# Kernel tuning notes

Measured on AMD Instinct MI355X. Metric: run time of the kernel, lower is better.

The kernel has to match this reference:

```python
import jax, jax.numpy as jnp
from jax import lax
import numpy as np

B, T, K = 256, 512, 256
MAX_SEQ = 512  # max_sequence_length; output padded to MAX_SEQ + 2


def setup_inputs() -> dict:
    key = jax.random.key(0)
    k1, k2 = jax.random.split(key)
    emissions = jax.random.normal(k1, (B, T, K), dtype=jnp.float32)
    transitions = jax.random.normal(k2, (K, K), dtype=jnp.float32)
    mask = jnp.ones((B, T), dtype=jnp.int32)  # prefix mask; here full-length
    return {"emissions": emissions, "transitions": transitions, "mask": mask,
            "max_sequence_length": MAX_SEQ}


def _crf_decode(emissions, transitions, mask):
    # emissions: [B, T, K] float; transitions: [K, K]; mask: [B, T] int (prefix 1s)
    b, t, k = emissions.shape
    state0 = emissions[:, 0, :]                      # [B, K]
    em_rest = jnp.swapaxes(emissions[:, 1:, :], 0, 1)  # [T-1, B, K]
    mk_rest = jnp.swapaxes(mask[:, 1:], 0, 1)           # [T-1, B]

    def fwd(state, xs):
        em_t, mk_t = xs
        # scores[b, i, j] = state[b, i] + transitions[i, j]  (prev tag i -> cur tag j)
        scores = state[:, :, None] + transitions[None, :, :]   # [B, K, K]
        bp = jnp.argmax(scores, axis=1).astype(jnp.int32)       # [B, K] best prev tag
        new_state = jnp.max(scores, axis=1) + em_t              # [B, K]
        valid = (mk_t > 0)[:, None]
        # RNN-with-mask semantics: keep last valid state past sequence end
        return jnp.where(valid, new_state, state), bp

    last_state, bps = lax.scan(fwd, state0, (em_rest, mk_rest))  # bps: [T-1, B, K]
    last_tag = jnp.argmax(last_state, axis=-1).astype(jnp.int32)  # [B]

    def bwd(tag, xs):
        bp_t, mk_t = xs
        out = tag  # tag at this timestep
        prev = jnp.take_along_axis(bp_t, tag[:, None], axis=1)[:, 0]
        tag = jnp.where(mk_t > 0, prev, tag)  # only step back on valid positions
        return tag, out

    tag0, outs = lax.scan(bwd, last_tag, (bps, mk_rest), reverse=True)
    # outs[t] = tag at position t+1 (t = 0..T-2); tag0 = tag at position 0
    tags = jnp.concatenate([tag0[:, None], jnp.swapaxes(outs, 0, 1)], axis=1)  # [B, T]
    return tags


def reference(emissions, transitions, mask, max_sequence_length):
    tags = _crf_decode(emissions, transitions, mask)
    tags = tags * mask  # zero out padding positions
    pad = max_sequence_length + 2 - tags.shape[1]
    return jnp.pad(tags, ((0, 0), (0, pad)))
```

## Files before the change

kernel.cpp:

```cpp
#include <hip/hip_runtime.h>


#define TK 256
#define TT 512

typedef float v2f __attribute__((ext_vector_type(2)));
typedef float v4f __attribute__((ext_vector_type(4)));

__device__ __forceinline__ float max3f(float a, float b, float c) {
  float d;
  asm("v_max3_f32 %0, %1, %2, %3" : "=v"(d) : "v"(a), "v"(b), "v"(c));
  return d;
}

__global__ void transpose_kernel(const float* __restrict__ trans,
                                 float* __restrict__ transT) {
  int j = blockIdx.x;
  int i = threadIdx.x;
  transT[(size_t)j * TK + i] = trans[(size_t)i * TK + j];
}

#define K16(X) X(0) X(1) X(2) X(3) X(4) X(5) X(6) X(7) \
               X(8) X(9) X(10) X(11) X(12) X(13) X(14) X(15)

__global__ __launch_bounds__(1024)
__attribute__((amdgpu_waves_per_eu(4, 4)))
void crf_fwd(const float* __restrict__ em,
             const float* __restrict__ transT,
             const int* __restrict__ mask,
             float* __restrict__ states) {
  const int b = blockIdx.x;
  const int tid = threadIdx.x;
  const int lane = tid & 63;
  const int w = tid >> 6;
  const int g = w >> 1;
  const int p = w & 1;
  const int j0 = 128 * p + 2 * lane;

  __shared__ __align__(16) float st_w[16][32];
  __shared__ float part[2][8][2][2][64];
  __shared__ int mk[TT];

  const float* ta = transT + (size_t)j0 * TK + 32 * g;
  const float* tbq = ta + TK;
#define TRD(n) \
  const v2f TA##n = *reinterpret_cast<const v2f*>(ta + 2 * (n)); \
  const v2f TB##n = *reinterpret_cast<const v2f*>(tbq + 2 * (n));
  K16(TRD)
#undef TRD

  if (tid < TT) mk[tid] = mask[(size_t)b * TT + tid];

  const size_t base = (size_t)b * TT * TK;
  const int pj = g >> 2;
  const int sel = lane & 1;
  const int col = 16 * (g & 3) + (lane >> 1);

  float ns = 0.f, e1 = 0.f, e2 = 0.f;
  if (lane < 32) {
    ns = em[base + 32 * g + lane];
    st_w[w][lane] = ns;
    if (p == 0) states[base + 32 * g + lane] = ns;
    e1 = em[base + TK + 32 * g + lane];
    e2 = em[base + 2 * TK + 32 * g + lane];
  }
  __syncthreads();

  const float* emp = em + base + 3 * TK + 32 * g + lane;
  float* stg = states + base + TK + 32 * g + lane;
  const float* sw = st_w[w];

  for (int t = 1; t < TT; ++t) {
    const v4f S0 = reinterpret_cast<const v4f*>(sw)[0];
    const v4f S1 = reinterpret_cast<const v4f*>(sw)[1];
    const v4f S2 = reinterpret_cast<const v4f*>(sw)[2];
    const v4f S3 = reinterpret_cast<const v4f*>(sw)[3];
    const v4f S4 = reinterpret_cast<const v4f*>(sw)[4];
    const v4f S5 = reinterpret_cast<const v4f*>(sw)[5];
    const v4f S6 = reinterpret_cast<const v4f*>(sw)[6];
    const v4f S7 = reinterpret_cast<const v4f*>(sw)[7];

    float ax, ay;
    {
      const float c0 = S0.x + TA0.x, c1 = S0.y + TA0.y;
      ax = fmaxf(c0, c1);
      const float d0 = S0.x + TB0.x, d1 = S0.y + TB0.y;
      ay = fmaxf(d0, d1);
    }
#define STEP2(Sa, Sb, TAn, TBn)                                   \
    {                                                             \
      const float c0 = Sa + TAn.x, c1 = Sb + TAn.y;               \
      ax = max3f(ax, c0, c1);                                     \
      const float d0 = Sa + TBn.x, d1 = Sb + TBn.y;               \
      ay = max3f(ay, d0, d1);                                     \
    }
    STEP2(S0.z, S0.w, TA1, TB1)
    STEP2(S1.x, S1.y, TA2, TB2)
    STEP2(S1.z, S1.w, TA3, TB3)
    STEP2(S2.x, S2.y, TA4, TB4)
    STEP2(S2.z, S2.w, TA5, TB5)
    STEP2(S3.x, S3.y, TA6, TB6)
    STEP2(S3.z, S3.w, TA7, TB7)
    STEP2(S4.x, S4.y, TA8, TB8)
    STEP2(S4.z, S4.w, TA9, TB9)
    STEP2(S5.x, S5.y, TA10, TB10)
    STEP2(S5.z, S5.w, TA11, TB11)
    STEP2(S6.x, S6.y, TA12, TB12)
    STEP2(S6.z, S6.w, TA13, TB13)
    STEP2(S7.x, S7.y, TA14, TB14)
    STEP2(S7.z, S7.w, TA15, TB15)
#undef STEP2

    float* pw = &part[t & 1][g][p][0][lane];
    pw[0] = ax;
    pw[64] = ay;

    __builtin_amdgcn_sched_barrier(0);
    asm volatile("s_waitcnt lgkmcnt(0)" ::: "memory");
    __builtin_amdgcn_s_barrier();
    __builtin_amdgcn_sched_barrier(0);

    if (lane < 32) {
      const float* pf = &part[t & 1][0][pj][sel][col];
      const float f0 = pf[0];
      const float f1 = pf[256];
      const float f2 = pf[512];
      const float f3 = pf[768];
      const float f4 = pf[1024];
      const float f5 = pf[1280];
      const float f6 = pf[1536];
      const float f7 = pf[1792];
      float f = max3f(fmaxf(f0, f1), f2, f3);
      f = max3f(f, f4, f5);
      f = max3f(f, f6, f7);
      ns = (mk[t] > 0) ? (f + e1) : ns;
      st_w[w][lane] = ns;
      if (p == 0) *stg = ns;
      stg += TK;
      e1 = e2;
      if (t + 2 < TT) e2 = *emp;
      emp += TK;
    }
  }
}

__device__ __forceinline__ float wave_max(float m) {
#pragma unroll
  for (int d = 1; d < 64; d <<= 1) m = fmaxf(m, __shfl_xor(m, d, 64));
  return m;
}

__device__ __forceinline__ int first_eq_idx(float s0, float s1, float s2,
                                            float s3, float m) {
  unsigned long long b0 = __ballot(s0 == m);
  unsigned long long b1 = __ballot(s1 == m);
  unsigned long long b2 = __ballot(s2 == m);
  unsigned long long b3 = __ballot(s3 == m);
  int best = 0x7fffffff;
  if (b0) best = min(best, 4 * (__ffsll(b0) - 1) + 0);
  if (b1) best = min(best, 4 * (__ffsll(b1) - 1) + 1);
  if (b2) best = min(best, 4 * (__ffsll(b2) - 1) + 2);
  if (b3) best = min(best, 4 * (__ffsll(b3) - 1) + 3);
  return best;
}

__global__ __launch_bounds__(64, 1) void crf_bwd(const float* __restrict__ states,
                                                 const float* __restrict__ transT,
                                                 const int* __restrict__ mask,
                                                 int* __restrict__ out,
                                                 int out_stride) {
  const int b = blockIdx.x;
  const int lane = threadIdx.x;

  __shared__ int mk[TT];
  for (int q = lane; q < TT; q += 64) mk[q] = mask[(size_t)b * TT + q];
  __syncthreads();

  const size_t sbase = (size_t)b * TT * TK;
  int* outp = out + (size_t)b * out_stride;

  for (int q = TT + lane; q < out_stride; q += 64) outp[q] = 0;

  const float* srow = states + sbase;
  float4 r = *reinterpret_cast<const float4*>(srow + (size_t)(TT - 1) * TK + 4 * lane);
  float lm = fmaxf(fmaxf(r.x, r.y), fmaxf(r.z, r.w));
  lm = wave_max(lm);
  int tag = first_eq_idx(r.x, r.y, r.z, r.w, lm);

  auto LOADROW = [&](int rr) -> float4 {
    return *reinterpret_cast<const float4*>(srow + (size_t)rr * TK + 4 * lane);
  };
  float4 p0 = LOADROW(TT - 2), p1 = LOADROW(TT - 3), p2 = LOADROW(TT - 4),
         p3 = LOADROW(TT - 5);

  auto STEP = [&](float4 pr, int t) {
    int mkt = mk[t];
    if (lane == 0) outp[t] = (mkt > 0) ? tag : 0;
    const float4 tv =
        *reinterpret_cast<const float4*>(transT + (size_t)tag * TK + 4 * lane);
    float s0 = pr.x + tv.x;
    float s1 = pr.y + tv.y;
    float s2 = pr.z + tv.z;
    float s3 = pr.w + tv.w;
    float m = fmaxf(fmaxf(s0, s1), fmaxf(s2, s3));
    m = wave_max(m);
    int prev = first_eq_idx(s0, s1, s2, s3, m);
    tag = (mkt > 0) ? prev : tag;
  };

  int t = TT - 1;
  while (t >= 4) {
    STEP(p0, t);     if (t - 5 >= 0) p0 = LOADROW(t - 5);
    STEP(p1, t - 1); if (t - 6 >= 0) p1 = LOADROW(t - 6);
    STEP(p2, t - 2); if (t - 7 >= 0) p2 = LOADROW(t - 7);
    STEP(p3, t - 3); if (t - 8 >= 0) p3 = LOADROW(t - 8);
    t -= 4;
  }
  STEP(p0, 3);
  STEP(p1, 2);
  STEP(p2, 1);
  if (lane == 0) outp[0] = (mk[0] > 0) ? tag : 0;
}

extern "C" void kernel_launch(void* const* d_in, const int* in_sizes, int n_in,
                              void* d_out, int out_size, void* d_ws, size_t ws_size,
                              hipStream_t stream) {
  const float* em = (const float*)d_in[0];
  const float* trans = (const float*)d_in[1];
  const int* mask = (const int*)d_in[2];
  int* out = (int*)d_out;

  const int B = in_sizes[0] / (TT * TK);
  const int out_stride = out_size / B;

  float* states = (float*)d_ws;
  float* transT = states + (size_t)B * TT * TK;

  transpose_kernel<<<TK, TK, 0, stream>>>(trans, transT);
  crf_fwd<<<B, 1024, 0, stream>>>(em, transT, mask, states);
  crf_bwd<<<B, 64, 0, stream>>>(states, transT, mask, out, out_stride);
}
```

Before: 794.4 us.

## Fuse CRF forward scan and backtrack into a single kernel

Merges the forward Viterbi kernel and the backtracking kernel into one launch: after the forward loop, wave 0 of each block does the backtrack over the states it just wrote, reusing the mask already staged in LDS. This removes a kernel launch and the gap between the two kernels, and may let the backtrack read recently written states from cache. It also drops the sched_barrier fences around the step barrier and rewrites the max3 inline asm as an accumulate form. The trade-off is that a 1024-thread block stays resident while only one wave does the serial backtrack, and the compiler is now freer to reorder around the barrier.

Result: no change. 794.3 us (-0.0%).

```diff
diff --git a/kernel.cpp b/kernel.cpp
--- a/kernel.cpp
+++ b/kernel.cpp
@@ -7,10 +7,8 @@
 typedef float v2f __attribute__((ext_vector_type(2)));
 typedef float v4f __attribute__((ext_vector_type(4)));
 
-__device__ __forceinline__ float max3f(float a, float b, float c) {
-  float d;
-  asm("v_max3_f32 %0, %1, %2, %3" : "=v"(d) : "v"(a), "v"(b), "v"(c));
-  return d;
+__device__ __forceinline__ void max3acc(float& acc, float a, float b) {
+  asm("v_max3_f32 %0, %0, %1, %2" : "+v"(acc) : "v"(a), "v"(b));
 }
 
 __global__ void transpose_kernel(const float* __restrict__ trans,
@@ -20,15 +18,34 @@
   transT[(size_t)j * TK + i] = trans[(size_t)i * TK + j];
 }
 
-#define K16(X) X(0) X(1) X(2) X(3) X(4) X(5) X(6) X(7) \
-               X(8) X(9) X(10) X(11) X(12) X(13) X(14) X(15)
+__device__ __forceinline__ float wave_max(float m) {
+#pragma unroll
+  for (int d = 1; d < 64; d <<= 1) m = fmaxf(m, __shfl_xor(m, d, 64));
+  return m;
+}
+
+__device__ __forceinline__ int first_eq_idx(float s0, float s1, float s2,
+                                            float s3, float m) {
+  unsigned long long b0 = __ballot(s0 == m);
+  unsigned long long b1 = __ballot(s1 == m);
+  unsigned long long b2 = __ballot(s2 == m);
+  unsigned long long b3 = __ballot(s3 == m);
+  int best = 0x7fffffff;
+  if (b0) best = min(best, 4 * (__ffsll(b0) - 1) + 0);
+  if (b1) best = min(best, 4 * (__ffsll(b1) - 1) + 1);
+  if (b2) best = min(best, 4 * (__ffsll(b2) - 1) + 2);
+  if (b3) best = min(best, 4 * (__ffsll(b3) - 1) + 3);
+  return best;
+}
 
 __global__ __launch_bounds__(1024)
 __attribute__((amdgpu_waves_per_eu(4, 4)))
-void crf_fwd(const float* __restrict__ em,
-             const float* __restrict__ transT,
-             const int* __restrict__ mask,
-             float* __restrict__ states) {
+void crf_fused(const float* __restrict__ em,
+               const float* __restrict__ transT,
+               const int* __restrict__ mask,
+               float* __restrict__ states,
+               int* __restrict__ out,
+               int out_stride) {
   const int b = blockIdx.x;
   const int tid = threadIdx.x;
   const int lane = tid & 63;
@@ -43,11 +60,14 @@
 
   const float* ta = transT + (size_t)j0 * TK + 32 * g;
   const float* tbq = ta + TK;
+#define K16(X) X(0) X(1) X(2) X(3) X(4) X(5) X(6) X(7) \
+               X(8) X(9) X(10) X(11) X(12) X(13) X(14) X(15)
 #define TRD(n) \
   const v2f TA##n = *reinterpret_cast<const v2f*>(ta + 2 * (n)); \
   const v2f TB##n = *reinterpret_cast<const v2f*>(tbq + 2 * (n));
   K16(TRD)
 #undef TRD
+#undef K16
 
   if (tid < TT) mk[tid] = mask[(size_t)b * TT + tid];
 
@@ -71,14 +91,15 @@
   const float* sw = st_w[w];
 
   for (int t = 1; t < TT; ++t) {
-    const v4f S0 = reinterpret_cast<const v4f*>(sw)[0];
-    const v4f S1 = reinterpret_cast<const v4f*>(sw)[1];
-    const v4f S2 = reinterpret_cast<const v4f*>(sw)[2];
-    const v4f S3 = reinterpret_cast<const v4f*>(sw)[3];
-    const v4f S4 = reinterpret_cast<const v4f*>(sw)[4];
-    const v4f S5 = reinterpret_cast<const v4f*>(sw)[5];
-    const v4f S6 = reinterpret_cast<const v4f*>(sw)[6];
-    const v4f S7 = reinterpret_cast<const v4f*>(sw)[7];
+    const v4f* swq = reinterpret_cast<const v4f*>(sw);
+    const v4f S0 = swq[0];
+    const v4f S1 = swq[1];
+    const v4f S2 = swq[2];
+    const v4f S3 = swq[3];
+    const v4f S4 = swq[4];
+    const v4f S5 = swq[5];
+    const v4f S6 = swq[6];
+    const v4f S7 = swq[7];
 
     float ax, ay;
     {
@@ -90,9 +111,9 @@
 #define STEP2(Sa, Sb, TAn, TBn)                                   \
     {                                                             \
       const float c0 = Sa + TAn.x, c1 = Sb + TAn.y;               \
-      ax = max3f(ax, c0, c1);                                     \
+      max3acc(ax, c0, c1);                                        \
       const float d0 = Sa + TBn.x, d1 = Sb + TBn.y;               \
-      ay = max3f(ay, d0, d1);                                     \
+      max3acc(ay, d0, d1);                                        \
     }
     STEP2(S0.z, S0.w, TA1, TB1)
     STEP2(S1.x, S1.y, TA2, TB2)
@@ -115,10 +136,8 @@
     pw[0] = ax;
     pw[64] = ay;
 
-    __builtin_amdgcn_sched_barrier(0);
     asm volatile("s_waitcnt lgkmcnt(0)" ::: "memory");
     __builtin_amdgcn_s_barrier();
-    __builtin_amdgcn_sched_barrier(0);
 
     if (lane < 32) {
       const float* pf = &part[t & 1][0][pj][sel][col];
@@ -130,9 +149,10 @@
       const float f5 = pf[1280];
       const float f6 = pf[1536];
       const float f7 = pf[1792];
-      float f = max3f(fmaxf(f0, f1), f2, f3);
-      f = max3f(f, f4, f5);
-      f = max3f(f, f6, f7);
+      float f = fmaxf(f0, f1);
+      max3acc(f, f2, f3);
+      max3acc(f, f4, f5);
+      max3acc(f, f6, f7);
       ns = (mk[t] > 0) ? (f + e1) : ns;
       st_w[w][lane] = ns;
       if (p == 0) *stg = ns;
@@ -142,43 +162,13 @@
       emp += TK;
     }
   }
-}
-
-__device__ __forceinline__ float wave_max(float m) {
-#pragma unroll
-  for (int d = 1; d < 64; d <<= 1) m = fmaxf(m, __shfl_xor(m, d, 64));
-  return m;
-}
-
-__device__ __forceinline__ int first_eq_idx(float s0, float s1, float s2,
-                                            float s3, float m) {
-  unsigned long long b0 = __ballot(s0 == m);
-  unsigned long long b1 = __ballot(s1 == m);
-  unsigned long long b2 = __ballot(s2 == m);
-  unsigned long long b3 = __ballot(s3 == m);
-  int best = 0x7fffffff;
-  if (b0) best = min(best, 4 * (__ffsll(b0) - 1) + 0);
-  if (b1) best = min(best, 4 * (__ffsll(b1) - 1) + 1);
-  if (b2) best = min(best, 4 * (__ffsll(b2) - 1) + 2);
-  if (b3) best = min(best, 4 * (__ffsll(b3) - 1) + 3);
-  return best;
-}
-
-__global__ __launch_bounds__(64, 1) void crf_bwd(const float* __restrict__ states,
-                                                 const float* __restrict__ transT,
-                                                 const int* __restrict__ mask,
-                                                 int* __restrict__ out,
-                                                 int out_stride) {
-  const int b = blockIdx.x;
-  const int lane = threadIdx.x;
-
-  __shared__ int mk[TT];
-  for (int q = lane; q < TT; q += 64) mk[q] = mask[(size_t)b * TT + q];
+
+  __threadfence_block();
   __syncthreads();
-
-  const size_t sbase = (size_t)b * TT * TK;
+  if (w != 0) return;
+
+  const size_t sbase = base;
   int* outp = out + (size_t)b * out_stride;
-
   for (int q = TT + lane; q < out_stride; q += 64) outp[q] = 0;
 
   const float* srow = states + sbase;
@@ -237,6 +227,5 @@
   float* transT = states + (size_t)B * TT * TK;
 
   transpose_kernel<<<TK, TK, 0, stream>>>(trans, transT);
-  crf_fwd<<<B, 1024, 0, stream>>>(em, transT, mask, states);
-  crf_bwd<<<B, 64, 0, stream>>>(states, transT, mask, out, out_stride);
-}
+  crf_fused<<<B, 1024, 0, stream>>>(em, transT, mask, states, out, out_stride);
+}
```
